# Optimization experiments

Hardware: AMD Instinct MI355X
Metric: run time of the kernel (lower is better)

## Reference

```python
import jax, jax.numpy as jnp
import numpy as np

IMG = 128; P = 16; ND = IMG // P; N = ND * ND  # 64 patches
INF = 3 * P * P      # 768 flattened patch features
ATT = 768; HID = 3072; OUT = 768; B = 64
EPS = 1e-5


def setup_inputs() -> dict:
    key = jax.random.key(0)
    ks = jax.random.split(key, 24)
    w = lambda k, shape: jax.random.normal(k, shape, jnp.float32) * 0.02
    return {
        "x": jax.random.normal(ks[0], (B, 3, IMG, IMG), jnp.float32),
        # per-patch q/k/v projections: [n, in, out] weights, [n, out] biases
        "Wq": w(ks[1], (N, INF, ATT)), "bq": w(ks[2], (N, ATT)),
        "Wk": w(ks[3], (N, INF, ATT)), "bk": w(ks[4], (N, ATT)),
        "Wv": w(ks[5], (N, INF, ATT)), "bv": w(ks[6], (N, ATT)),
        "ln_g": jnp.ones((ATT,), jnp.float32), "ln_b": jnp.zeros((ATT,), jnp.float32),
        "p1_w": w(ks[7], (INF, ATT)), "p1_b": w(ks[8], (ATT,)),
        "w0": w(ks[9], (ATT, HID)),  "b0": w(ks[10], (HID,)),
        "w1": w(ks[11], (HID, HID)), "b1": w(ks[12], (HID,)),
        "w2": w(ks[13], (HID, HID)), "b2": w(ks[14], (HID,)),
        "w3": w(ks[15], (HID, HID)), "b3": w(ks[16], (HID,)),
        "w4": w(ks[17], (HID, OUT)), "b4": w(ks[18], (OUT,)),
        "p2_w": w(ks[19], (ATT, OUT)), "p2_b": w(ks[20], (OUT,)),
    }


def _forward(x, Wq, bq, Wk, bk, Wv, bv, ln_g, ln_b, p1_w, p1_b,
             w0, b0, w1, b1, w2, b2, w3, b3, w4, b4, p2_w, p2_b):
    b_ = x.shape[0]
    # patch split (row-major over (i,j) blocks) then flatten channel*patch dims
    flat = x.reshape(b_, 3, ND, P, ND, P).transpose(0, 2, 4, 1, 3, 5).reshape(b_, N, INF)
    # per-patch projections, attention taken ACROSS the batch dim (as in source)
    q = jnp.einsum('bnf,nfd->bnd', flat, Wq) + bq
    k = jnp.einsum('bnf,nfd->bnd', flat, Wk) + bk
    v = jnp.einsum('bnf,nfd->bnd', flat, Wv) + bv
    scores = jnp.einsum('bnd,cnd->nbc', q, k) / jnp.sqrt(jnp.float32(ATT))  # [n,B,B]
    attn = jnp.einsum('nbc,cnd->bnd', jax.nn.softmax(scores, axis=-1), v)  # [B,n,ATT]
    # LayerNorm(att_features)
    mu = attn.mean(-1, keepdims=True)
    var = ((attn - mu) ** 2).mean(-1, keepdims=True)
    ln = (attn - mu) / jnp.sqrt(var + EPS) * ln_g + ln_b
    att = ln + flat @ p1_w + p1_b
    # linear stack (no nonlinearity in the source)
    h = att @ w0 + b0
    h = h @ w1 + b1
    h = h @ w2 + b2
    h = h @ w3 + b3
    h = h @ w4 + b4
    proj = h + att @ p2_w + p2_b
    return jax.nn.softmax(proj, axis=2)


def reference(x, Wq, bq, Wk, bk, Wv, bv, ln_g, ln_b, p1_w, p1_b,
              w0, b0, w1, b1, w2, b2, w3, b3, w4, b4, p2_w, p2_b):
    return _forward(x, Wq, bq, Wk, bk, Wv, bv, ln_g, ln_b, p1_w, p1_b,
                    w0, b0, w1, b1, w2, b2, w3, b3, w4, b4, p2_w, p2_b)
```

## Files before the change

kernel.cpp:

```cpp
#include <hip/hip_runtime.h>
#include <hip/hip_bf16.h>

using bf16 = __bf16;
using bf16x4 = __bf16 __attribute__((ext_vector_type(4)));
using bf16x8 = __bf16 __attribute__((ext_vector_type(8)));
using f32x4 = float __attribute__((ext_vector_type(4)));

static constexpr long ROWEL = 64L * 768;

__global__ __launch_bounds__(256) void k_patchify(const float* __restrict__ x, bf16* __restrict__ flat)
{
    const int n = blockIdx.x;
    const int b = blockIdx.y;
    const int i_ = n >> 3, j_ = n & 7;
    for (int it = 0; it < 3; ++it) {
        int f = threadIdx.x + it * 256;
        int c = f >> 8, rem = f & 255, pi = rem >> 4, pj = rem & 15;
        float v = x[(((long)(b * 3 + c)) << 14) + ((i_ * 16 + pi) << 7) + (j_ * 16 + pj)];
        flat[(long)b * ROWEL + n * 768 + f] = (bf16)v;
    }
}

__global__ __launch_bounds__(256) void k_cvt_t2(
    const float* __restrict__ W0, bf16* __restrict__ T0,
    const float* __restrict__ W1, bf16* __restrict__ T1)
{
    const int z = blockIdx.z;
    const float* W = z ? W1 : W0;
    bf16* Wt = z ? T1 : T0;
    const int Kd = z ? 768 : 3072, Nd = 768;
    if (z && blockIdx.x >= 12) return;
    __shared__ bf16 T[64 * 66];
    const int k0 = blockIdx.x * 64, n0 = blockIdx.y * 64;
    const int tid = threadIdx.x;
    const int kr = tid >> 4, nc = (tid & 15) * 4;
#pragma unroll
    for (int i = 0; i < 4; ++i) {
        f32x4 v = *(const f32x4*)(W + (long)(k0 + kr + i * 16) * Nd + n0 + nc);
#pragma unroll
        for (int e = 0; e < 4; ++e)
            T[(kr + i * 16) * 66 + nc + e] = (bf16)v[e];
    }
    __syncthreads();
    const int nr = tid >> 3, ks = (tid & 7) * 8;
#pragma unroll
    for (int it = 0; it < 2; ++it) {
        int n = nr + it * 32;
        bf16x8 o;
#pragma unroll
        for (int j = 0; j < 8; ++j) o[j] = T[(ks + j) * 66 + n];
        *(bf16x8*)(Wt + (long)(n0 + n) * Kd + k0 + ks) = o;
    }
}

__global__ __launch_bounds__(256) void k_cast4(
    const float* __restrict__ s0, bf16* __restrict__ d0,
    const float* __restrict__ s1, bf16* __restrict__ d1,
    const float* __restrict__ s2, bf16* __restrict__ d2,
    const float* __restrict__ s3, bf16* __restrict__ d3)
{
    const int z = blockIdx.y;
    const float* W = z == 0 ? s0 : z == 1 ? s1 : z == 2 ? s2 : s3;
    bf16* o = z == 0 ? d0 : z == 1 ? d1 : z == 2 ? d2 : d3;
    const long nelem = z == 0 ? 768L * 3072 : 3072L * 3072;
    long i = ((long)blockIdx.x * 256 + threadIdx.x) * 8;
    if (i >= nelem) return;
    f32x4 a = *(const f32x4*)(W + i);
    f32x4 b = *(const f32x4*)(W + i + 4);
    bf16x8 v;
#pragma unroll
    for (int e = 0; e < 4; ++e) { v[e] = (bf16)a[e]; v[4 + e] = (bf16)b[e]; }
    *(bf16x8*)(o + i) = v;
}

__device__ __forceinline__ void barrier_lgkm()
{
    asm volatile("s_waitcnt lgkmcnt(0)" ::: "memory");
    __builtin_amdgcn_s_barrier();
    __builtin_amdgcn_sched_barrier(0);
}

template<int BM, int BN>
__global__ __launch_bounds__(256) void k_gemm_rs(
    const bf16* __restrict__ A, long lda,
    const bf16* __restrict__ Bt, long ldb,
    int Ks,
    const float* __restrict__ bias,
    const float* __restrict__ addm,
    bf16* __restrict__ Cb, float* __restrict__ Cf, long ldc,
    float* __restrict__ Cp, long zstride)
{
    constexpr int WM = BM / 2, WN = BN / 2, FM = WM / 16, FN = WN / 16;
    constexpr int NA = BM / 64, NB = BN / 64;
    __shared__ bf16 As[2][BM * 32];
    __shared__ bf16 Bs[2][BN * 32];
    const int tid = threadIdx.x, lane = tid & 63, wave = tid >> 6;
    const int wm = wave >> 1, wn = wave & 1;
    const long m0 = (long)blockIdx.x * BM, n0 = (long)blockIdx.y * BN;
    const long kofs = (long)blockIdx.z * Ks;

    f32x4 acc[FM][FN];
#pragma unroll
    for (int i = 0; i < FM; ++i)
#pragma unroll
        for (int j = 0; j < FN; ++j) acc[i][j] = (f32x4){0.f, 0.f, 0.f, 0.f};

    const int nk = Ks >> 5;
    bf16x8 Xa[NA], Xb[NB], Ya[NA], Yb[NB];

    auto LOAD = [&](bf16x8 (&ra)[NA], bf16x8 (&rb)[NB], int kt) {
        const long kb = kofs + (long)kt * 32;
#pragma unroll
        for (int i = 0; i < NA; ++i) {
            const int c = i * 256 + tid, r = c >> 2, sg = c & 3;
            ra[i] = *(const bf16x8*)(A + (m0 + r) * lda + kb + sg * 8);
        }
#pragma unroll
        for (int i = 0; i < NB; ++i) {
            const int c = i * 256 + tid, r = c >> 2, sg = c & 3;
            rb[i] = *(const bf16x8*)(Bt + (n0 + r) * ldb + kb + sg * 8);
        }
    };
    auto WRITE = [&](bf16x8 (&ra)[NA], bf16x8 (&rb)[NB], int buf) {
#pragma unroll
        for (int i = 0; i < NA; ++i)
            *(bf16x8*)&As[buf][(i * 256 + tid) * 8] = ra[i];
#pragma unroll
        for (int i = 0; i < NB; ++i)
            *(bf16x8*)&Bs[buf][(i * 256 + tid) * 8] = rb[i];
    };
    auto COMPUTE = [&](int buf) {
        bf16x8 af[FM], bfr[FN];
#pragma unroll
        for (int i = 0; i < FM; ++i)
            af[i] = *(const bf16x8*)&As[buf][(wm * WM + i * 16 + (lane & 15)) * 32 + (lane >> 4) * 8];
#pragma unroll
        for (int j = 0; j < FN; ++j)
            bfr[j] = *(const bf16x8*)&Bs[buf][(wn * WN + j * 16 + (lane & 15)) * 32 + (lane >> 4) * 8];
#pragma unroll
        for (int i = 0; i < FM; ++i)
#pragma unroll
            for (int j = 0; j < FN; ++j)
                acc[i][j] = __builtin_amdgcn_mfma_f32_16x16x32_bf16(af[i], bfr[j], acc[i][j], 0, 0, 0);
    };

    LOAD(Xa, Xb, 0);
    LOAD(Ya, Yb, 1);
    WRITE(Xa, Xb, 0);
    barrier_lgkm();
    for (int t = 0; t < nk; t += 2) {
        if (t + 2 < nk) LOAD(Xa, Xb, t + 2);
        COMPUTE(0);
        if (t + 1 < nk) WRITE(Ya, Yb, 1);
        barrier_lgkm();
        if (t + 1 < nk) {
            if (t + 3 < nk) LOAD(Ya, Yb, t + 3);
            COMPUTE(1);
            if (t + 2 < nk) WRITE(Xa, Xb, 0);
            barrier_lgkm();
        }
    }

    if (Cp) {
        float* Cz = Cp + (long)blockIdx.z * zstride;
#pragma unroll
        for (int j = 0; j < FN; ++j) {
            const long col = n0 + wn * WN + j * 16 + (lane & 15);
#pragma unroll
            for (int i = 0; i < FM; ++i)
#pragma unroll
                for (int r = 0; r < 4; ++r) {
                    const long row = m0 + wm * WM + i * 16 + (lane >> 4) * 4 + r;
                    Cz[row * ldc + col] = acc[i][j][r];
                }
        }
        return;
    }
#pragma unroll
    for (int j = 0; j < FN; ++j) {
        const long col = n0 + wn * WN + j * 16 + (lane & 15);
        const float bb = bias ? bias[col] : 0.f;
#pragma unroll
        for (int i = 0; i < FM; ++i) {
#pragma unroll
            for (int r = 0; r < 4; ++r) {
                const long row = m0 + wm * WM + i * 16 + (lane >> 4) * 4 + r;
                const long idx = row * ldc + col;
                float v = acc[i][j][r] + bb;
                if (addm) v += addm[idx];
                if (Cb) Cb[idx] = (bf16)v;
                if (Cf) Cf[idx] = v;
            }
        }
    }
}

__global__ __launch_bounds__(256) void k_qkv(
    const bf16* __restrict__ flat,
    const float* __restrict__ Wq, const float* __restrict__ Wk, const float* __restrict__ Wv,
    const float* __restrict__ bq, const float* __restrict__ bk, const float* __restrict__ bv,
    bf16* __restrict__ qo, bf16* __restrict__ ko, bf16* __restrict__ vo)
{
    const int zz = blockIdx.z;
    const float* W = zz == 0 ? Wq : zz == 1 ? Wk : Wv;
    const float* bias = zz == 0 ? bq : zz == 1 ? bk : bv;
    bf16* out = zz == 0 ? qo : zz == 1 ? ko : vo;

    __shared__ bf16 As[2][64 * 32];
    __shared__ bf16 Bs[2][64 * 32];
    const int tid = threadIdx.x, lane = tid & 63, wave = tid >> 6;
    const int wm = wave >> 1, wn = wave & 1;
    const int n0 = blockIdx.x * 64;
    const int z = blockIdx.y;
    const float* Wz = W + (long)z * 589824;

    f32x4 acc[2][2];
#pragma unroll
    for (int i = 0; i < 2; ++i)
#pragma unroll
        for (int j = 0; j < 2; ++j) acc[i][j] = (f32x4){0.f, 0.f, 0.f, 0.f};

    const int bcol = tid & 63;
    const int bkg = (tid >> 6) * 8;
    bf16x8 Xa, Ya;
    float Xb[8], Yb[8];

    auto LOAD = [&](bf16x8& ra, float (&rb)[8], int kt) {
        const int kb = kt * 32;
        const int r = tid >> 2, sg = tid & 3;
        ra = *(const bf16x8*)(flat + (long)r * ROWEL + z * 768 + kb + sg * 8);
#pragma unroll
        for (int e = 0; e < 8; ++e)
            rb[e] = Wz[(long)(kb + bkg + e) * 768 + n0 + bcol];
    };
    auto WRITE = [&](bf16x8& ra, float (&rb)[8], int buf) {
        *(bf16x8*)&As[buf][tid * 8] = ra;
        bf16x8 bb;
#pragma unroll
        for (int e = 0; e < 8; ++e) bb[e] = (bf16)rb[e];
        *(bf16x8*)&Bs[buf][bcol * 32 + bkg] = bb;
    };
    auto COMPUTE = [&](int buf) {
        bf16x8 af[2], bfr[2];
#pragma unroll
        for (int i = 0; i < 2; ++i)
            af[i] = *(const bf16x8*)&As[buf][(wm * 32 + i * 16 + (lane & 15)) * 32 + (lane >> 4) * 8];
#pragma unroll
        for (int j = 0; j < 2; ++j)
            bfr[j] = *(const bf16x8*)&Bs[buf][(wn * 32 + j * 16 + (lane & 15)) * 32 + (lane >> 4) * 8];
#pragma unroll
        for (int i = 0; i < 2; ++i)
#pragma unroll
            for (int j = 0; j < 2; ++j)
                acc[i][j] = __builtin_amdgcn_mfma_f32_16x16x32_bf16(af[i], bfr[j], acc[i][j], 0, 0, 0);
    };

    const int nk = 24;
    LOAD(Xa, Xb, 0);
    LOAD(Ya, Yb, 1);
    WRITE(Xa, Xb, 0);
    barrier_lgkm();
    for (int t = 0; t < nk; t += 2) {
        if (t + 2 < nk) LOAD(Xa, Xb, t + 2);
        COMPUTE(0);
        if (t + 1 < nk) WRITE(Ya, Yb, 1);
        barrier_lgkm();
        if (t + 1 < nk) {
            if (t + 3 < nk) LOAD(Ya, Yb, t + 3);
            COMPUTE(1);
            if (t + 2 < nk) WRITE(Xa, Xb, 0);
            barrier_lgkm();
        }
    }

#pragma unroll
    for (int j = 0; j < 2; ++j) {
        const int col = n0 + wn * 32 + j * 16 + (lane & 15);
        const float bb = bias[z * 768 + col];
#pragma unroll
        for (int i = 0; i < 2; ++i) {
#pragma unroll
            for (int r = 0; r < 4; ++r) {
                const int row = wm * 32 + i * 16 + (lane >> 4) * 4 + r;
                out[(long)row * ROWEL + z * 768 + col] = (bf16)(acc[i][j][r] + bb);
            }
        }
    }
}

__global__ __launch_bounds__(256) void k_skadd(
    const float* __restrict__ P, long zstride, int S, long nelem, bf16* __restrict__ out)
{
    long i = ((long)blockIdx.x * 256 + threadIdx.x) * 4;
    if (i >= nelem) return;
    f32x4 s = *(const f32x4*)(P + i);
    for (int z = 1; z < S; ++z) {
        f32x4 p = *(const f32x4*)(P + (long)z * zstride + i);
        s += p;
    }
    bf16x4 o;
#pragma unroll
    for (int e = 0; e < 4; ++e) o[e] = (bf16)s[e];
    *(bf16x4*)(out + i) = o;
}

__global__ __launch_bounds__(256) void k_skaddT(
    const float* __restrict__ P, long zstride, int S,
    const float* __restrict__ p2w, bf16* __restrict__ Mt)
{
    const int n = blockIdx.x;
    for (int k = threadIdx.x; k < 768; k += 256) {
        float s = p2w[(long)k * 768 + n];
        for (int z = 0; z < S; ++z) s += P[(long)z * zstride + n * 768 + k];
        Mt[n * 768 + k] = (bf16)s;
    }
}

template<typename TW>
__global__ __launch_bounds__(256) void k_vm2(
    const float* __restrict__ Pin, const float* __restrict__ bin, const TW* __restrict__ W,
    int K, int N, float* __restrict__ Pout)
{
    __shared__ float red[4][64];
    const int tid = threadIdx.x;
    const int nl = tid & 63, kq = tid >> 6;
    const int n = blockIdx.x * 64 + nl;
    const int kc = blockIdx.y;
    const int kchunk = K / 8, kslice = kchunk / 4;
    const int k0 = kc * kchunk + kq * kslice;
    float acc = 0.f;
#pragma unroll 4
    for (int k = k0; k < k0 + kslice; ++k) {
        float vk = bin[k];
        if (Pin) {
#pragma unroll
            for (int j = 0; j < 8; ++j) vk += Pin[(long)j * K + k];
        }
        acc += vk * (float)W[(long)k * N + n];
    }
    red[kq][nl] = acc;
    __syncthreads();
    if (kq == 0)
        Pout[(long)kc * N + n] = red[0][nl] + red[1][nl] + red[2][nl] + red[3][nl];
}

__global__ __launch_bounds__(256) void k_vred(
    const float* __restrict__ P, const float* __restrict__ b1, const float* __restrict__ b2,
    int N, float* __restrict__ out)
{
    const int n = blockIdx.x * 256 + threadIdx.x;
    if (n >= N) return;
    float s = b1[n] + (b2 ? b2[n] : 0.f);
#pragma unroll
    for (int j = 0; j < 8; ++j) s += P[(long)j * N + n];
    out[n] = s;
}

__global__ __launch_bounds__(256) void k_attn(
    const bf16* __restrict__ q, const bf16* __restrict__ k, const bf16* __restrict__ v,
    float* __restrict__ attn)
{
    const int dc = blockIdx.x;
    const int n = blockIdx.y;
    __shared__ bf16 QT[64 * 72];
    __shared__ bf16 KT[64 * 72];
    __shared__ float S[64 * 66];
    __shared__ bf16 P[64 * 72];
    __shared__ bf16 VT[128 * 72];

    const int tid = threadIdx.x, lane = tid & 63, wave = tid >> 6;
    const int wm = wave >> 1, wn = wave & 1;

    f32x4 accs[2][2];
#pragma unroll
    for (int i = 0; i < 2; ++i)
#pragma unroll
        for (int j = 0; j < 2; ++j) accs[i][j] = (f32x4){0.f, 0.f, 0.f, 0.f};

    for (int kt = 0; kt < 12; ++kt) {
#pragma unroll
        for (int i = 0; i < 2; ++i) {
            int cid = tid + i * 256;
            int r = cid >> 3, seg = cid & 7;
            *(bf16x8*)&QT[r * 72 + seg * 8] = *(const bf16x8*)(q + (long)r * ROWEL + n * 768 + kt * 64 + seg * 8);
            *(bf16x8*)&KT[r * 72 + seg * 8] = *(const bf16x8*)(k + (long)r * ROWEL + n * 768 + kt * 64 + seg * 8);
        }
        __syncthreads();
#pragma unroll
        for (int ks = 0; ks < 2; ++ks) {
            bf16x8 qa[2], kb2[2];
#pragma unroll
            for (int i = 0; i < 2; ++i)
                qa[i] = *(const bf16x8*)&QT[(wm * 32 + i * 16 + (lane & 15)) * 72 + ks * 32 + (lane >> 4) * 8];
#pragma unroll
            for (int j = 0; j < 2; ++j)
                kb2[j] = *(const bf16x8*)&KT[(wn * 32 + j * 16 + (lane & 15)) * 72 + ks * 32 + (lane >> 4) * 8];
#pragma unroll
            for (int i = 0; i < 2; ++i)
#pragma unroll
                for (int j = 0; j < 2; ++j)
                    accs[i][j] = __builtin_amdgcn_mfma_f32_16x16x32_bf16(qa[i], kb2[j], accs[i][j], 0, 0, 0);
        }
        __syncthreads();
    }
    const float sc = 0.03608439182435161f;
#pragma unroll
    for (int i = 0; i < 2; ++i)
#pragma unroll
        for (int j = 0; j < 2; ++j)
#pragma unroll
            for (int r = 0; r < 4; ++r)
                S[(wm * 32 + i * 16 + (lane >> 4) * 4 + r) * 66 + wn * 32 + j * 16 + (lane & 15)] = accs[i][j][r] * sc;
    __syncthreads();

    {
        int r = tid >> 2, l4 = tid & 3;
        float m = -1e30f;
        for (int c = l4; c < 64; c += 4) m = fmaxf(m, S[r * 66 + c]);
        m = fmaxf(m, __shfl_xor(m, 1));
        m = fmaxf(m, __shfl_xor(m, 2));
        float s = 0.f;
// ... 61 lines not shown
    for (int c = 0; c < 3; ++c) {
        xv[c] = *(const f32x4*)(p + c * 256 + lane * 4);
        s += xv[c][0] + xv[c][1] + xv[c][2] + xv[c][3];
    }
#pragma unroll
    for (int o = 1; o < 64; o <<= 1) s += __shfl_xor(s, o);
    const float mu = s * (1.f / 768.f);
    float vs = 0.f;
#pragma unroll
    for (int c = 0; c < 3; ++c)
#pragma unroll
        for (int e = 0; e < 4; ++e) { float d = xv[c][e] - mu; vs += d * d; }
#pragma unroll
    for (int o = 1; o < 64; o <<= 1) vs += __shfl_xor(vs, o);
    const float rstd = rsqrtf(vs * (1.f / 768.f) + 1e-5f);
#pragma unroll
    for (int c = 0; c < 3; ++c)
#pragma unroll
        for (int e = 0; e < 4; ++e) {
            int col = c * 256 + lane * 4 + e;
            p[col] = (xv[c][e] - mu) * rstd * g[col] + bb[col];
        }
}

__global__ __launch_bounds__(256) void k_softmax(float* __restrict__ o)
{
    const long row = blockIdx.x * 4 + (threadIdx.x >> 6);
    const int lane = threadIdx.x & 63;
    float* p = o + row * 768;
    f32x4 xv[3];
    float m = -1e30f;
#pragma unroll
    for (int c = 0; c < 3; ++c) {
        xv[c] = *(const f32x4*)(p + c * 256 + lane * 4);
        m = fmaxf(m, fmaxf(fmaxf(xv[c][0], xv[c][1]), fmaxf(xv[c][2], xv[c][3])));
    }
#pragma unroll
    for (int o2 = 1; o2 < 64; o2 <<= 1) m = fmaxf(m, __shfl_xor(m, o2));
    float s = 0.f;
#pragma unroll
    for (int c = 0; c < 3; ++c)
#pragma unroll
        for (int e = 0; e < 4; ++e) { float ev = __expf(xv[c][e] - m); xv[c][e] = ev; s += ev; }
#pragma unroll
    for (int o2 = 1; o2 < 64; o2 <<= 1) s += __shfl_xor(s, o2);
    const float inv = 1.f / s;
#pragma unroll
    for (int c = 0; c < 3; ++c)
        *(f32x4*)(p + c * 256 + lane * 4) = xv[c] * inv;
}

extern "C" void kernel_launch(void* const* d_in, const int* in_sizes, int n_in,
                              void* d_out, int out_size, void* d_ws, size_t ws_size,
                              hipStream_t stream)
{
    const float* x   = (const float*)d_in[0];
    const float* Wq  = (const float*)d_in[1];
    const float* bq  = (const float*)d_in[2];
    const float* Wk  = (const float*)d_in[3];
    const float* bk  = (const float*)d_in[4];
    const float* Wv  = (const float*)d_in[5];
    const float* bv  = (const float*)d_in[6];
    const float* lng = (const float*)d_in[7];
    const float* lnb = (const float*)d_in[8];
    const float* p1w = (const float*)d_in[9];
    const float* p1b = (const float*)d_in[10];
    const float* w0  = (const float*)d_in[11];
    const float* b0  = (const float*)d_in[12];
    const float* w1  = (const float*)d_in[13];
    const float* b1  = (const float*)d_in[14];
    const float* w2  = (const float*)d_in[15];
    const float* b2  = (const float*)d_in[16];
    const float* w3  = (const float*)d_in[17];
    const float* b3  = (const float*)d_in[18];
    const float* w4  = (const float*)d_in[19];
    const float* b4  = (const float*)d_in[20];
    const float* p2w = (const float*)d_in[21];
    const float* p2b = (const float*)d_in[22];
    float* out = (float*)d_out;

    char* wsbase = (char*)d_ws;
    size_t off = 0;
    auto alloc = [&](size_t bytes) { char* p = wsbase + off; off += (bytes + 255) & ~(size_t)255; return p; };
    bf16*  flat = (bf16*)alloc(4096L * 768 * 2);
    bf16*  qb   = (bf16*)alloc(4096L * 768 * 2);
    bf16*  kb   = (bf16*)alloc(4096L * 768 * 2);
    bf16*  vb2  = (bf16*)alloc(4096L * 768 * 2);
    float* attn = (float*)alloc(4096L * 768 * 4);
    bf16*  att  = (bf16*)alloc(4096L * 768 * 2);
    bf16*  p1t  = (bf16*)alloc(768L * 768 * 2);
    bf16*  w4t  = (bf16*)alloc(768L * 3072 * 2);
    bf16*  w0c  = (bf16*)alloc(768L * 3072 * 2);
    bf16*  w1c  = (bf16*)alloc(3072L * 3072 * 2);
    bf16*  w2c  = (bf16*)alloc(3072L * 3072 * 2);
    bf16*  w3c  = (bf16*)alloc(3072L * 3072 * 2);
    bf16*  M1   = (bf16*)alloc(768L * 3072 * 2);
    bf16*  M2   = (bf16*)alloc(768L * 3072 * 2);
    bf16*  M3   = (bf16*)alloc(768L * 3072 * 2);
    bf16*  Mt   = (bf16*)alloc(768L * 768 * 2);
    float* Cp   = (float*)alloc(6L * 768 * 3072 * 4);
    float* vPa  = (float*)alloc(8L * 3072 * 4);
    float* vPb  = (float*)alloc(8L * 3072 * 4);
    float* c4   = (float*)alloc(768 * 4);
    if (off > ws_size) return;

    const long ZS = 768L * 3072;
    const long ZS4 = 768L * 768;

    k_patchify<<<dim3(64, 64), 256, 0, stream>>>(x, flat);
    k_cast4<<<dim3(4608, 4), 256, 0, stream>>>(w0, w0c, w1, w1c, w2, w2c, w3, w3c);
    k_cvt_t2<<<dim3(48, 12, 2), 256, 0, stream>>>(w4, w4t, p1w, p1t);

    k_qkv<<<dim3(12, 64, 3), 256, 0, stream>>>(flat, Wq, Wk, Wv, bq, bk, bv, qb, kb, vb2);

    k_attn<<<dim3(6, 64), 256, 0, stream>>>(qb, kb, vb2, attn);
    k_ln<<<1024, 256, 0, stream>>>(attn, lng, lnb);
    k_gemm_rs<64, 64><<<dim3(64, 12), 256, 0, stream>>>(flat, 768, p1t, 768, 768, p1b, attn, att, nullptr, 768, nullptr, 0);

    k_gemm_rs<64, 64><<<dim3(12, 48, 3), 256, 0, stream>>>(w4t, 3072, w3c, 3072, 1024, nullptr, nullptr, nullptr, nullptr, 3072, Cp, ZS);
    k_skadd<<<2304, 256, 0, stream>>>(Cp, ZS, 3, ZS, M1);
    k_gemm_rs<64, 64><<<dim3(12, 48, 3), 256, 0, stream>>>(M1, 3072, w2c, 3072, 1024, nullptr, nullptr, nullptr, nullptr, 3072, Cp, ZS);
    k_skadd<<<2304, 256, 0, stream>>>(Cp, ZS, 3, ZS, M2);
    k_gemm_rs<64, 64><<<dim3(12, 48, 3), 256, 0, stream>>>(M2, 3072, w1c, 3072, 1024, nullptr, nullptr, nullptr, nullptr, 3072, Cp, ZS);
    k_skadd<<<2304, 256, 0, stream>>>(Cp, ZS, 3, ZS, M3);
    k_gemm_rs<64, 64><<<dim3(12, 12, 6), 256, 0, stream>>>(M3, 3072, w0c, 3072, 512, nullptr, nullptr, nullptr, nullptr, 768, Cp, ZS4);
    k_skaddT<<<768, 256, 0, stream>>>(Cp, ZS4, 6, p2w, Mt);

    k_vm2<bf16><<<dim3(48, 8), 256, 0, stream>>>(nullptr, b0, w1c, 3072, 3072, vPa);
    k_vm2<bf16><<<dim3(48, 8), 256, 0, stream>>>(vPa, b1, w2c, 3072, 3072, vPb);
    k_vm2<bf16><<<dim3(48, 8), 256, 0, stream>>>(vPb, b2, w3c, 3072, 3072, vPa);
    k_vm2<float><<<dim3(12, 8), 256, 0, stream>>>(vPa, b3, w4, 3072, 768, vPb);
    k_vred<<<3, 256, 0, stream>>>(vPb, b4, p2b, 768, c4);

    k_gemm_rs<64, 64><<<dim3(64, 12), 256, 0, stream>>>(att, 768, Mt, 768, 768, c4, nullptr, nullptr, out, 768, nullptr, 0);
    k_softmax<<<1024, 256, 0, stream>>>(out);
}
```

Before: 577.5 us.

## Fuse weight casts and split-K reductions into chained GEMM loads with XCD-aware block mapping

Measured after the change: 684.7 us. +18.6%, slower.

```diff
diff --git a/kernel.cpp b/kernel.cpp
--- a/kernel.cpp
+++ b/kernel.cpp
@@ -53,26 +53,6 @@
     }
 }
 
-__global__ __launch_bounds__(256) void k_cast4(
-    const float* __restrict__ s0, bf16* __restrict__ d0,
-    const float* __restrict__ s1, bf16* __restrict__ d1,
-    const float* __restrict__ s2, bf16* __restrict__ d2,
-    const float* __restrict__ s3, bf16* __restrict__ d3)
-{
-    const int z = blockIdx.y;
-    const float* W = z == 0 ? s0 : z == 1 ? s1 : z == 2 ? s2 : s3;
-    bf16* o = z == 0 ? d0 : z == 1 ? d1 : z == 2 ? d2 : d3;
-    const long nelem = z == 0 ? 768L * 3072 : 3072L * 3072;
-    long i = ((long)blockIdx.x * 256 + threadIdx.x) * 8;
-    if (i >= nelem) return;
-    f32x4 a = *(const f32x4*)(W + i);
-    f32x4 b = *(const f32x4*)(W + i + 4);
-    bf16x8 v;
-#pragma unroll
-    for (int e = 0; e < 4; ++e) { v[e] = (bf16)a[e]; v[4 + e] = (bf16)b[e]; }
-    *(bf16x8*)(o + i) = v;
-}
-
 __device__ __forceinline__ void barrier_lgkm()
 {
     asm volatile("s_waitcnt lgkmcnt(0)" ::: "memory");
@@ -87,8 +67,7 @@
     int Ks,
     const float* __restrict__ bias,
     const float* __restrict__ addm,
-    bf16* __restrict__ Cb, float* __restrict__ Cf, long ldc,
-    float* __restrict__ Cp, long zstride)
+    bf16* __restrict__ Cb, float* __restrict__ Cf, long ldc)
 {
     constexpr int WM = BM / 2, WN = BN / 2, FM = WM / 16, FN = WN / 16;
     constexpr int NA = BM / 64, NB = BN / 64;
@@ -97,7 +76,6 @@
     const int tid = threadIdx.x, lane = tid & 63, wave = tid >> 6;
     const int wm = wave >> 1, wn = wave & 1;
     const long m0 = (long)blockIdx.x * BM, n0 = (long)blockIdx.y * BN;
-    const long kofs = (long)blockIdx.z * Ks;
 
     f32x4 acc[FM][FN];
 #pragma unroll
@@ -109,7 +87,7 @@
     bf16x8 Xa[NA], Xb[NB], Ya[NA], Yb[NB];
 
     auto LOAD = [&](bf16x8 (&ra)[NA], bf16x8 (&rb)[NB], int kt) {
-        const long kb = kofs + (long)kt * 32;
+        const long kb = (long)kt * 32;
 #pragma unroll
         for (int i = 0; i < NA; ++i) {
             const int c = i * 256 + tid, r = c >> 2, sg = c & 3;
@@ -161,21 +139,6 @@
         }
     }
 
-    if (Cp) {
-        float* Cz = Cp + (long)blockIdx.z * zstride;
-#pragma unroll
-        for (int j = 0; j < FN; ++j) {
-            const long col = n0 + wn * WN + j * 16 + (lane & 15);
-#pragma unroll
-            for (int i = 0; i < FM; ++i)
-#pragma unroll
-                for (int r = 0; r < 4; ++r) {
-                    const long row = m0 + wm * WM + i * 16 + (lane >> 4) * 4 + r;
-                    Cz[row * ldc + col] = acc[i][j][r];
-                }
-        }
-        return;
-    }
 #pragma unroll
     for (int j = 0; j < FN; ++j) {
         const long col = n0 + wn * WN + j * 16 + (lane & 15);
@@ -195,24 +158,151 @@
     }
 }
 
+template<bool ASUM>
+__global__ __launch_bounds__(256) void k_chain(
+    const bf16* __restrict__ Abf, const float* __restrict__ Ap, long apz, long lda,
+    const float* __restrict__ Bf, long ldb,
+    int Ks, int NX, int NY,
+    float* __restrict__ Cp, long zstride, long ldc)
+{
+    constexpr int BM = 64, BN = 64;
+    constexpr int WM = 32, WN = 32, FM = 2, FN = 2;
+    __shared__ bf16 As[2][BM * 32];
+    __shared__ bf16 Bs[2][BN * 32];
+    const int tid = threadIdx.x, lane = tid & 63, wave = tid >> 6;
+    const int wm = wave >> 1, wn = wave & 1;
+    const int gid = blockIdx.x;
+    const int xcd = gid & 7, mm = gid >> 3;
+    const int bx = mm % NX, u = mm / NX;
+    const int p = 8 * u + xcd;
+    const int by = p % NY, bz = p / NY;
+    const long m0 = (long)bx * BM, n0 = (long)by * BN;
+    const long kofs = (long)bz * Ks;
+
+    f32x4 acc[FM][FN];
+#pragma unroll
+    for (int i = 0; i < FM; ++i)
+#pragma unroll
+        for (int j = 0; j < FN; ++j) acc[i][j] = (f32x4){0.f, 0.f, 0.f, 0.f};
+
+    const int nk = Ks >> 5;
+
+    bf16x8 XaB, YaB;
+    f32x4 Xa[2][3], Ya[2][3];
+    f32x4 Xb[2], Yb[2];
+
+    auto LOAD = [&](bf16x8& raB, f32x4 (&ra)[2][3], f32x4 (&rb)[2], int kt) {
+        const long kb = kofs + (long)kt * 32;
+        if (ASUM) {
+#pragma unroll
+            for (int i = 0; i < 2; ++i) {
+                const int c = i * 256 + tid, r = c >> 3, k4 = (c & 7) * 4;
+#pragma unroll
+                for (int z = 0; z < 3; ++z)
+                    ra[i][z] = *(const f32x4*)(Ap + (long)z * apz + (m0 + r) * lda + kb + k4);
+            }
+        } else {
+            const int r = tid >> 2, sg = tid & 3;
+            raB = *(const bf16x8*)(Abf + (m0 + r) * lda + kb + sg * 8);
+        }
+#pragma unroll
+        for (int i = 0; i < 2; ++i) {
+            const int c = i * 256 + tid, n = c >> 3, k4 = (c & 7) * 4;
+            rb[i] = *(const f32x4*)(Bf + (n0 + n) * ldb + kb + k4);
+        }
+    };
+    auto WRITE = [&](bf16x8& raB, f32x4 (&ra)[2][3], f32x4 (&rb)[2], int buf) {
+        if (ASUM) {
+#pragma unroll
+            for (int i = 0; i < 2; ++i) {
+                const int c = i * 256 + tid, r = c >> 3, k4 = (c & 7) * 4;
+                f32x4 s = ra[i][0] + ra[i][1] + ra[i][2];
+                bf16x4 o;
+#pragma unroll
+                for (int e = 0; e < 4; ++e) o[e] = (bf16)s[e];
+                *(bf16x4*)&As[buf][r * 32 + k4] = o;
+            }
+        } else {
+            *(bf16x8*)&As[buf][tid * 8] = raB;
+        }
+#pragma unroll
+        for (int i = 0; i < 2; ++i) {
+            const int c = i * 256 + tid, n = c >> 3, k4 = (c & 7) * 4;
+            bf16x4 o;
+#pragma unroll
+            for (int e = 0; e < 4; ++e) o[e] = (bf16)rb[i][e];
+            *(bf16x4*)&Bs[buf][n * 32 + k4] = o;
+        }
+    };
+    auto COMPUTE = [&](int buf) {
+        bf16x8 af[FM], bfr[FN];
+#pragma unroll
+        for (int i = 0; i < FM; ++i)
+            af[i] = *(const bf16x8*)&As[buf][(wm * WM + i * 16 + (lane & 15)) * 32 + (lane >> 4) * 8];
+#pragma unroll
+        for (int j = 0; j < FN; ++j)
+            bfr[j] = *(const bf16x8*)&Bs[buf][(wn * WN + j * 16 + (lane & 15)) * 32 + (lane >> 4) * 8];
+#pragma unroll
+        for (int i = 0; i < FM; ++i)
+#pragma unroll
+            for (int j = 0; j < FN; ++j)
+                acc[i][j] = __builtin_amdgcn_mfma_f32_16x16x32_bf16(af[i], bfr[j], acc[i][j], 0, 0, 0);
+    };
+
+    LOAD(XaB, Xa, Xb, 0);
+    LOAD(YaB, Ya, Yb, 1);
+    WRITE(XaB, Xa, Xb, 0);
+    barrier_lgkm();
+    for (int t = 0; t < nk; t += 2) {
+        if (t + 2 < nk) LOAD(XaB, Xa, Xb, t + 2);
+        COMPUTE(0);
+        if (t + 1 < nk) WRITE(YaB, Ya, Yb, 1);
+        barrier_lgkm();
+        if (t + 1 < nk) {
+            if (t + 3 < nk) LOAD(YaB, Ya, Yb, t + 3);
+            COMPUTE(1);
+            if (t + 2 < nk) WRITE(XaB, Xa, Xb, 0);
+            barrier_lgkm();
+        }
+    }
+
+    float* Cz = Cp + (long)bz * zstride;
+#pragma unroll
+    for (int j = 0; j < FN; ++j) {
+        const long col = n0 + wn * WN + j * 16 + (lane & 15);
+#pragma unroll
+        for (int i = 0; i < FM; ++i)
+#pragma unroll
+            for (int r = 0; r < 4; ++r) {
+                const long row = m0 + wm * WM + i * 16 + (lane >> 4) * 4 + r;
+                Cz[row * ldc + col] = acc[i][j][r];
+            }
+    }
+}
+
 __global__ __launch_bounds__(256) void k_qkv(
     const bf16* __restrict__ flat,
     const float* __restrict__ Wq, const float* __restrict__ Wk, const float* __restrict__ Wv,
     const float* __restrict__ bq, const float* __restrict__ bk, const float* __restrict__ bv,
     bf16* __restrict__ qo, bf16* __restrict__ ko, bf16* __restrict__ vo)
 {
-    const int zz = blockIdx.z;
-    const float* W = zz == 0 ? Wq : zz == 1 ? Wk : Wv;
-    const float* bias = zz == 0 ? bq : zz == 1 ? bk : bv;
-    bf16* out = zz == 0 ? qo : zz == 1 ? ko : vo;
+    const int gid = blockIdx.x;
+    const int xcd = gid & 7, mm = gid >> 3;
+    const int nt = mm % 12, u = mm / 12;
+    const int p = 8 * u + xcd;
+    const int z = p >> 6;
+    const int zp = p & 63;
+
+    const float* W = z == 0 ? Wq : z == 1 ? Wk : Wv;
+    const float* bias = z == 0 ? bq : z == 1 ? bk : bv;
+    bf16* out = z == 0 ? qo : z == 1 ? ko : vo;
 
     __shared__ bf16 As[2][64 * 32];
     __shared__ bf16 Bs[2][64 * 32];
     const int tid = threadIdx.x, lane = tid & 63, wave = tid >> 6;
     const int wm = wave >> 1, wn = wave & 1;
-    const int n0 = blockIdx.x * 64;
-    const int z = blockIdx.y;
-    const float* Wz = W + (long)z * 589824;
+    const int n0 = nt * 64;
+    const float* Wz = W + (long)zp * 589824;
 
     f32x4 acc[2][2];
 #pragma unroll
@@ -222,25 +312,25 @@
 
     const int bcol = tid & 63;
     const int bkg = (tid >> 6) * 8;
-    bf16x8 Xa, Ya;
-    float Xb[8], Yb[8];
-
-    auto LOAD = [&](bf16x8& ra, float (&rb)[8], int kt) {
+    bf16x8 A0, A1, A2, A3;
+    float B0[8], B1[8], B2[8], B3[8];
+
+    auto LOADQ = [&](bf16x8& ra, float (&rb)[8], int kt) {
         const int kb = kt * 32;
         const int r = tid >> 2, sg = tid & 3;
-        ra = *(const bf16x8*)(flat + (long)r * ROWEL + z * 768 + kb + sg * 8);
+        ra = *(const bf16x8*)(flat + (long)r * ROWEL + zp * 768 + kb + sg * 8);
 #pragma unroll
         for (int e = 0; e < 8; ++e)
             rb[e] = Wz[(long)(kb + bkg + e) * 768 + n0 + bcol];
     };
-    auto WRITE = [&](bf16x8& ra, float (&rb)[8], int buf) {
+    auto WRITEQ = [&](bf16x8& ra, float (&rb)[8], int buf) {
         *(bf16x8*)&As[buf][tid * 8] = ra;
         bf16x8 bb;
 #pragma unroll
         for (int e = 0; e < 8; ++e) bb[e] = (bf16)rb[e];
         *(bf16x8*)&Bs[buf][bcol * 32 + bkg] = bb;
     };
-    auto COMPUTE = [&](int buf) {
+    auto COMPUTEQ = [&](int buf) {
         bf16x8 af[2], bfr[2];
 #pragma unroll
         for (int i = 0; i < 2; ++i)
@@ -256,52 +346,43 @@
     };
 
     const int nk = 24;
-    LOAD(Xa, Xb, 0);
-    LOAD(Ya, Yb, 1);
-    WRITE(Xa, Xb, 0);
+    LOADQ(A0, B0, 0);
+    LOADQ(A1, B1, 1);
+    LOADQ(A2, B2, 2);
+    WRITEQ(A0, B0, 0);
     barrier_lgkm();
-    for (int t = 0; t < nk; t += 2) {
-        if (t + 2 < nk) LOAD(Xa, Xb, t + 2);
-        COMPUTE(0);
-        if (t + 1 < nk) WRITE(Ya, Yb, 1);
+    for (int t = 0; t < nk; t += 4) {
+        if (t + 3 < nk) LOADQ(A3, B3, t + 3);
+        COMPUTEQ(0);
+        WRITEQ(A1, B1, 1);
         barrier_lgkm();
-        if (t + 1 < nk) {
-            if (t + 3 < nk) LOAD(Ya, Yb, t + 3);
-            COMPUTE(1);
-            if (t + 2 < nk) WRITE(Xa, Xb, 0);
-            barrier_lgkm();
-        }
+        if (t + 4 < nk) LOADQ(A0, B0, t + 4);
+        COMPUTEQ(1);
+        WRITEQ(A2, B2, 0);
+        barrier_lgkm();
+        if (t + 5 < nk) LOADQ(A1, B1, t + 5);
+        COMPUTEQ(0);
+        WRITEQ(A3, B3, 1);
+        barrier_lgkm();
+        if (t + 6 < nk) LOADQ(A2, B2, t + 6);
+        COMPUTEQ(1);
+        if (t + 4 < nk) WRITEQ(A0, B0, 0);
+        barrier_lgkm();
     }
 
 #pragma unroll
     for (int j = 0; j < 2; ++j) {
         const int col = n0 + wn * 32 + j * 16 + (lane & 15);
-        const float bb = bias[z * 768 + col];
+        const float bb = bias[zp * 768 + col];
 #pragma unroll
         for (int i = 0; i < 2; ++i) {
 #pragma unroll
             for (int r = 0; r < 4; ++r) {
                 const int row = wm * 32 + i * 16 + (lane >> 4) * 4 + r;
-                out[(long)row * ROWEL + z * 768 + col] = (bf16)(acc[i][j][r] + bb);
+                out[(long)row * ROWEL + zp * 768 + col] = (bf16)(acc[i][j][r] + bb);
             }
         }
     }
-}
-
-__global__ __launch_bounds__(256) void k_skadd(
-    const float* __restrict__ P, long zstride, int S, long nelem, bf16* __restrict__ out)
-{
-    long i = ((long)blockIdx.x * 256 + threadIdx.x) * 4;
-    if (i >= nelem) return;
-    f32x4 s = *(const f32x4*)(P + i);
-    for (int z = 1; z < S; ++z) {
-        f32x4 p = *(const f32x4*)(P + (long)z * zstride + i);
-        s += p;
-    }
-    bf16x4 o;
-#pragma unroll
-    for (int e = 0; e < 4; ++e) o[e] = (bf16)s[e];
-    *(bf16x4*)(out + i) = o;
 }
 
 __global__ __launch_bounds__(256) void k_skaddT(
@@ -316,9 +397,8 @@
     }
 }
 
-template<typename TW>
 __global__ __launch_bounds__(256) void k_vm2(
-    const float* __restrict__ Pin, const float* __restrict__ bin, const TW* __restrict__ W,
+    const float* __restrict__ Pin, const float* __restrict__ bin, const float* __restrict__ W,
     int K, int N, float* __restrict__ Pout)
 {
     __shared__ float red[4][64];
@@ -336,7 +416,7 @@
 #pragma unroll
             for (int j = 0; j < 8; ++j) vk += Pin[(long)j * K + k];
         }
-        acc += vk * (float)W[(long)k * N + n];
+        acc += vk * W[(long)k * N + n];
     }
     red[kq][nl] = acc;
     __syncthreads();
@@ -572,48 +652,38 @@
     bf16*  att  = (bf16*)alloc(4096L * 768 * 2);
     bf16*  p1t  = (bf16*)alloc(768L * 768 * 2);
     bf16*  w4t  = (bf16*)alloc(768L * 3072 * 2);
-    bf16*  w0c  = (bf16*)alloc(768L * 3072 * 2);
-    bf16*  w1c  = (bf16*)alloc(3072L * 3072 * 2);
-    bf16*  w2c  = (bf16*)alloc(3072L * 3072 * 2);
-    bf16*  w3c  = (bf16*)alloc(3072L * 3072 * 2);
-    bf16*  M1   = (bf16*)alloc(768L * 3072 * 2);
-    bf16*  M2   = (bf16*)alloc(768L * 3072 * 2);
-    bf16*  M3   = (bf16*)alloc(768L * 3072 * 2);
     bf16*  Mt   = (bf16*)alloc(768L * 768 * 2);
-    float* Cp   = (float*)alloc(6L * 768 * 3072 * 4);
+    float* Cpa  = (float*)alloc(3L * 768 * 3072 * 4);
+    float* Cpb  = (float*)alloc(6L * 768 * 768 * 4 > 3L * 768 * 3072 * 4 ? 6L * 768 * 768 * 4 : 3L * 768 * 3072 * 4);
     float* vPa  = (float*)alloc(8L * 3072 * 4);
     float* vPb  = (float*)alloc(8L * 3072 * 4);
     float* c4   = (float*)alloc(768 * 4);
     if (off > ws_size) return;
 
-    const long ZS = 768L * 3072;
+    const long ZS  = 768L * 3072;
     const long ZS4 = 768L * 768;
 
     k_patchify<<<dim3(64, 64), 256, 0, stream>>>(x, flat);
-    k_cast4<<<dim3(4608, 4), 256, 0, stream>>>(w0, w0c, w1, w1c, w2, w2c, w3, w3c);
     k_cvt_t2<<<dim3(48, 12, 2), 256, 0, stream>>>(w4, w4t, p1w, p1t);
 
-    k_qkv<<<dim3(12, 64, 3), 256, 0, stream>>>(flat, Wq, Wk, Wv, bq, bk, bv, qb, kb, vb2);
+    k_qkv<<<2304, 256, 0, stream>>>(flat, Wq, Wk, Wv, bq, bk, bv, qb, kb, vb2);
 
     k_attn<<<dim3(6, 64), 256, 0, stream>>>(qb, kb, vb2, attn);
     k_ln<<<1024, 256, 0, stream>>>(attn, lng, lnb);
-    k_gemm_rs<64, 64><<<dim3(64, 12), 256, 0, stream>>>(flat, 768, p1t, 768, 768, p1b, attn, att, nullptr, 768, nullptr, 0);
-
-    k_gemm_rs<64, 64><<<dim3(12, 48, 3), 256, 0, stream>>>(w4t, 3072, w3c, 3072, 1024, nullptr, nullptr, nullptr, nullptr, 3072, Cp, ZS);
-    k_skadd<<<2304, 256, 0, stream>>>(Cp, ZS, 3, ZS, M1);
-    k_gemm_rs<64, 64><<<dim3(12, 48, 3), 256, 0, stream>>>(M1, 3072, w2c, 3072, 1024, nullptr, nullptr, nullptr, nullptr, 3072, Cp, ZS);
-    k_skadd<<<2304, 256, 0, stream>>>(Cp, ZS, 3, ZS, M2);
-    k_gemm_rs<64, 64><<<dim3(12, 48, 3), 256, 0, stream>>>(M2, 3072, w1c, 3072, 1024, nullptr, nullptr, nullptr, nullptr, 3072, Cp, ZS);
-    k_skadd<<<2304, 256, 0, stream>>>(Cp, ZS, 3, ZS, M3);
-    k_gemm_rs<64, 64><<<dim3(12, 12, 6), 256, 0, stream>>>(M3, 3072, w0c, 3072, 512, nullptr, nullptr, nullptr, nullptr, 768, Cp, ZS4);
-    k_skaddT<<<768, 256, 0, stream>>>(Cp, ZS4, 6, p2w, Mt);
-
-    k_vm2<bf16><<<dim3(48, 8), 256, 0, stream>>>(nullptr, b0, w1c, 3072, 3072, vPa);
-    k_vm2<bf16><<<dim3(48, 8), 256, 0, stream>>>(vPa, b1, w2c, 3072, 3072, vPb);
-    k_vm2<bf16><<<dim3(48, 8), 256, 0, stream>>>(vPb, b2, w3c, 3072, 3072, vPa);
-    k_vm2<float><<<dim3(12, 8), 256, 0, stream>>>(vPa, b3, w4, 3072, 768, vPb);
+    k_gemm_rs<64, 64><<<dim3(64, 12), 256, 0, stream>>>(flat, 768, p1t, 768, 768, p1b, attn, att, nullptr, 768);
+
+    k_chain<false><<<1728, 256, 0, stream>>>(w4t, nullptr, 0, 3072, w3, 3072, 1024, 12, 48, Cpa, ZS, 3072);
+    k_chain<true><<<1728, 256, 0, stream>>>(nullptr, Cpa, ZS, 3072, w2, 3072, 1024, 12, 48, Cpb, ZS, 3072);
+    k_chain<true><<<1728, 256, 0, stream>>>(nullptr, Cpb, ZS, 3072, w1, 3072, 1024, 12, 48, Cpa, ZS, 3072);
+    k_chain<true><<<864, 256, 0, stream>>>(nullptr, Cpa, ZS, 3072, w0, 3072, 512, 12, 12, Cpb, ZS4, 768);
+    k_skaddT<<<768, 256, 0, stream>>>(Cpb, ZS4, 6, p2w, Mt);
+
+    k_vm2<<<dim3(48, 8), 256, 0, stream>>>(nullptr, b0, w1, 3072, 3072, vPa);
+    k_vm2<<<dim3(48, 8), 256, 0, stream>>>(vPa, b1, w2, 3072, 3072, vPb);
+    k_vm2<<<dim3(48, 8), 256, 0, stream>>>(vPb, b2, w3, 3072, 3072, vPa);
+    k_vm2<<<dim3(12, 8), 256, 0, stream>>>(vPa, b3, w4, 3072, 768, vPb);
     k_vred<<<3, 256, 0, stream>>>(vPb, b4, p2b, 768, c4);
 
-    k_gemm_rs<64, 64><<<dim3(64, 12), 256, 0, stream>>>(att, 768, Mt, 768, 768, c4, nullptr, nullptr, out, 768, nullptr, 0);
+    k_gemm_rs<64, 64><<<dim3(64, 12), 256, 0, stream>>>(att, 768, Mt, 768, 768, c4, nullptr, nullptr, out, 768);
     k_softmax<<<1024, 256, 0, stream>>>(out);
 }
```

## Add patch-major flat copy, XCD-aware QKV scheduling, and fewer split-K slices

Applied to the files above, without the earlier changes.

Measured after the change: 556.7 us. -3.6%, faster.

```diff
diff --git a/kernel.cpp b/kernel.cpp
--- a/kernel.cpp
+++ b/kernel.cpp
@@ -8,7 +8,8 @@
 
 static constexpr long ROWEL = 64L * 768;
 
-__global__ __launch_bounds__(256) void k_patchify(const float* __restrict__ x, bf16* __restrict__ flat)
+__global__ __launch_bounds__(256) void k_patchify(const float* __restrict__ x,
+                                                  bf16* __restrict__ flat, bf16* __restrict__ flat_nb)
 {
     const int n = blockIdx.x;
     const int b = blockIdx.y;
@@ -17,7 +18,9 @@
         int f = threadIdx.x + it * 256;
         int c = f >> 8, rem = f & 255, pi = rem >> 4, pj = rem & 15;
         float v = x[(((long)(b * 3 + c)) << 14) + ((i_ * 16 + pi) << 7) + (j_ * 16 + pj)];
-        flat[(long)b * ROWEL + n * 768 + f] = (bf16)v;
+        bf16 o = (bf16)v;
+        flat[(long)b * ROWEL + n * 768 + f] = o;
+        flat_nb[(long)n * ROWEL + b * 768 + f] = o;
     }
 }
 
@@ -87,8 +90,7 @@
     int Ks,
     const float* __restrict__ bias,
     const float* __restrict__ addm,
-    bf16* __restrict__ Cb, float* __restrict__ Cf, long ldc,
-    float* __restrict__ Cp, long zstride)
+    bf16* __restrict__ Cb, float* __restrict__ Cf, long ldc)
 {
     constexpr int WM = BM / 2, WN = BN / 2, FM = WM / 16, FN = WN / 16;
     constexpr int NA = BM / 64, NB = BN / 64;
@@ -97,7 +99,6 @@
     const int tid = threadIdx.x, lane = tid & 63, wave = tid >> 6;
     const int wm = wave >> 1, wn = wave & 1;
     const long m0 = (long)blockIdx.x * BM, n0 = (long)blockIdx.y * BN;
-    const long kofs = (long)blockIdx.z * Ks;
 
     f32x4 acc[FM][FN];
 #pragma unroll
@@ -109,7 +110,7 @@
     bf16x8 Xa[NA], Xb[NB], Ya[NA], Yb[NB];
 
     auto LOAD = [&](bf16x8 (&ra)[NA], bf16x8 (&rb)[NB], int kt) {
-        const long kb = kofs + (long)kt * 32;
+        const long kb = (long)kt * 32;
 #pragma unroll
         for (int i = 0; i < NA; ++i) {
             const int c = i * 256 + tid, r = c >> 2, sg = c & 3;
@@ -161,21 +162,6 @@
         }
     }
 
-    if (Cp) {
-        float* Cz = Cp + (long)blockIdx.z * zstride;
-#pragma unroll
-        for (int j = 0; j < FN; ++j) {
-            const long col = n0 + wn * WN + j * 16 + (lane & 15);
-#pragma unroll
-            for (int i = 0; i < FM; ++i)
-#pragma unroll
-                for (int r = 0; r < 4; ++r) {
-                    const long row = m0 + wm * WM + i * 16 + (lane >> 4) * 4 + r;
-                    Cz[row * ldc + col] = acc[i][j][r];
-                }
-        }
-        return;
-    }
 #pragma unroll
     for (int j = 0; j < FN; ++j) {
         const long col = n0 + wn * WN + j * 16 + (lane & 15);
@@ -195,24 +181,18 @@
     }
 }
 
-__global__ __launch_bounds__(256) void k_qkv(
-    const bf16* __restrict__ flat,
-    const float* __restrict__ Wq, const float* __restrict__ Wk, const float* __restrict__ Wv,
-    const float* __restrict__ bq, const float* __restrict__ bk, const float* __restrict__ bv,
-    bf16* __restrict__ qo, bf16* __restrict__ ko, bf16* __restrict__ vo)
-{
-    const int zz = blockIdx.z;
-    const float* W = zz == 0 ? Wq : zz == 1 ? Wk : Wv;
-    const float* bias = zz == 0 ? bq : zz == 1 ? bk : bv;
-    bf16* out = zz == 0 ? qo : zz == 1 ? ko : vo;
-
+__global__ __launch_bounds__(256) void k_chainrs(
+    const bf16* __restrict__ A, long lda,
+    const bf16* __restrict__ Bt, long ldb,
+    int Ks,
+    float* __restrict__ Cp, long zstride, long ldc)
+{
     __shared__ bf16 As[2][64 * 32];
     __shared__ bf16 Bs[2][64 * 32];
     const int tid = threadIdx.x, lane = tid & 63, wave = tid >> 6;
     const int wm = wave >> 1, wn = wave & 1;
-    const int n0 = blockIdx.x * 64;
-    const int z = blockIdx.y;
-    const float* Wz = W + (long)z * 589824;
+    const long m0 = (long)blockIdx.x * 64, n0 = (long)blockIdx.y * 64;
+    const long kofs = (long)blockIdx.z * Ks;
 
     f32x4 acc[2][2];
 #pragma unroll
@@ -220,25 +200,18 @@
 #pragma unroll
         for (int j = 0; j < 2; ++j) acc[i][j] = (f32x4){0.f, 0.f, 0.f, 0.f};
 
-    const int bcol = tid & 63;
-    const int bkg = (tid >> 6) * 8;
-    bf16x8 Xa, Ya;
-    float Xb[8], Yb[8];
-
-    auto LOAD = [&](bf16x8& ra, float (&rb)[8], int kt) {
-        const int kb = kt * 32;
+    const int nk = Ks >> 5;
+    bf16x8 Xa, Xb, Ya, Yb;
+
+    auto LOAD = [&](bf16x8& ra, bf16x8& rb, int kt) {
+        const long kb = kofs + (long)kt * 32;
         const int r = tid >> 2, sg = tid & 3;
-        ra = *(const bf16x8*)(flat + (long)r * ROWEL + z * 768 + kb + sg * 8);
-#pragma unroll
-        for (int e = 0; e < 8; ++e)
-            rb[e] = Wz[(long)(kb + bkg + e) * 768 + n0 + bcol];
-    };
-    auto WRITE = [&](bf16x8& ra, float (&rb)[8], int buf) {
+        ra = *(const bf16x8*)(A + (m0 + r) * lda + kb + sg * 8);
+        rb = *(const bf16x8*)(Bt + (n0 + r) * ldb + kb + sg * 8);
+    };
+    auto WRITE = [&](bf16x8& ra, bf16x8& rb, int buf) {
         *(bf16x8*)&As[buf][tid * 8] = ra;
-        bf16x8 bb;
-#pragma unroll
-        for (int e = 0; e < 8; ++e) bb[e] = (bf16)rb[e];
-        *(bf16x8*)&Bs[buf][bcol * 32 + bkg] = bb;
+        *(bf16x8*)&Bs[buf][tid * 8] = rb;
     };
     auto COMPUTE = [&](int buf) {
         bf16x8 af[2], bfr[2];
@@ -255,7 +228,6 @@
                 acc[i][j] = __builtin_amdgcn_mfma_f32_16x16x32_bf16(af[i], bfr[j], acc[i][j], 0, 0, 0);
     };
 
-    const int nk = 24;
     LOAD(Xa, Xb, 0);
     LOAD(Ya, Yb, 1);
     WRITE(Xa, Xb, 0);
@@ -273,16 +245,114 @@
         }
     }
 
+    float* Cz = Cp + (long)blockIdx.z * zstride;
+#pragma unroll
+    for (int j = 0; j < 2; ++j) {
+        const long col = n0 + wn * 32 + j * 16 + (lane & 15);
+#pragma unroll
+        for (int i = 0; i < 2; ++i)
+#pragma unroll
+            for (int r = 0; r < 4; ++r) {
+                const long row = m0 + wm * 32 + i * 16 + (lane >> 4) * 4 + r;
+                Cz[row * ldc + col] = acc[i][j][r];
+            }
+    }
+}
+
+__global__ __launch_bounds__(256) void k_qkv(
+    const bf16* __restrict__ flat_nb,
+    const float* __restrict__ Wq, const float* __restrict__ Wk, const float* __restrict__ Wv,
+    const float* __restrict__ bq, const float* __restrict__ bk, const float* __restrict__ bv,
+    bf16* __restrict__ qo, bf16* __restrict__ ko, bf16* __restrict__ vo)
+{
+    const int gid = blockIdx.x;
+    const int xcd = gid & 7, mm = gid >> 3;
+    const int nt = mm % 12, u = mm / 12;
+    const int p = 8 * u + xcd;
+    const int z = p >> 6;
+    const int zp = p & 63;
+
+    const float* W = z == 0 ? Wq : z == 1 ? Wk : Wv;
+    const float* bias = z == 0 ? bq : z == 1 ? bk : bv;
+    bf16* out = z == 0 ? qo : z == 1 ? ko : vo;
+
+    __shared__ bf16 As[2][64 * 32];
+    __shared__ bf16 Bs[2][64 * 32];
+    const int tid = threadIdx.x, lane = tid & 63, wave = tid >> 6;
+    const int wm = wave >> 1, wn = wave & 1;
+    const int n0 = nt * 64;
+    const float* Wz = W + (long)zp * 589824;
+    const bf16* Az = flat_nb + (long)zp * ROWEL;
+
+    f32x4 acc[2][2];
+#pragma unroll
+    for (int i = 0; i < 2; ++i)
+#pragma unroll
+        for (int j = 0; j < 2; ++j) acc[i][j] = (f32x4){0.f, 0.f, 0.f, 0.f};
+
+    const int bcol = tid & 63;
+    const int bkg = (tid >> 6) * 8;
+    bf16x8 Xa, Ya;
+    float Xb[8], Yb[8];
+
+    auto LOADQ = [&](bf16x8& ra, float (&rb)[8], int kt) {
+        const int kb = kt * 32;
+        const int r = tid >> 2, sg = tid & 3;
+        ra = *(const bf16x8*)(Az + (long)r * 768 + kb + sg * 8);
+#pragma unroll
+        for (int e = 0; e < 8; ++e)
+            rb[e] = Wz[(long)(kb + bkg + e) * 768 + n0 + bcol];
+    };
+    auto WRITEQ = [&](bf16x8& ra, float (&rb)[8], int buf) {
+        *(bf16x8*)&As[buf][tid * 8] = ra;
+        bf16x8 bb;
+#pragma unroll
+        for (int e = 0; e < 8; ++e) bb[e] = (bf16)rb[e];
+        *(bf16x8*)&Bs[buf][bcol * 32 + bkg] = bb;
+    };
+    auto COMPUTEQ = [&](int buf) {
+        bf16x8 af[2], bfr[2];
+#pragma unroll
+        for (int i = 0; i < 2; ++i)
+            af[i] = *(const bf16x8*)&As[buf][(wm * 32 + i * 16 + (lane & 15)) * 32 + (lane >> 4) * 8];
+#pragma unroll
+        for (int j = 0; j < 2; ++j)
+            bfr[j] = *(const bf16x8*)&Bs[buf][(wn * 32 + j * 16 + (lane & 15)) * 32 + (lane >> 4) * 8];
+#pragma unroll
+        for (int i = 0; i < 2; ++i)
+#pragma unroll
+            for (int j = 0; j < 2; ++j)
+                acc[i][j] = __builtin_amdgcn_mfma_f32_16x16x32_bf16(af[i], bfr[j], acc[i][j], 0, 0, 0);
+    };
+
+    const int nk = 24;
+    LOADQ(Xa, Xb, 0);
+    LOADQ(Ya, Yb, 1);
+    WRITEQ(Xa, Xb, 0);
+    barrier_lgkm();
+    for (int t = 0; t < nk; t += 2) {
+        if (t + 2 < nk) LOADQ(Xa, Xb, t + 2);
+        COMPUTEQ(0);
+        if (t + 1 < nk) WRITEQ(Ya, Yb, 1);
+        barrier_lgkm();
+        if (t + 1 < nk) {
+            if (t + 3 < nk) LOADQ(Ya, Yb, t + 3);
+            COMPUTEQ(1);
+            if (t + 2 < nk) WRITEQ(Xa, Xb, 0);
+            barrier_lgkm();
+        }
+    }
+
 #pragma unroll
     for (int j = 0; j < 2; ++j) {
         const int col = n0 + wn * 32 + j * 16 + (lane & 15);
-        const float bb = bias[z * 768 + col];
+        const float bb = bias[zp * 768 + col];
 #pragma unroll
         for (int i = 0; i < 2; ++i) {
 #pragma unroll
             for (int r = 0; r < 4; ++r) {
                 const int row = wm * 32 + i * 16 + (lane >> 4) * 4 + r;
-                out[(long)row * ROWEL + z * 768 + col] = (bf16)(acc[i][j][r] + bb);
+                out[(long)row * ROWEL + zp * 768 + col] = (bf16)(acc[i][j][r] + bb);
             }
         }
     }
@@ -564,7 +634,8 @@
     char* wsbase = (char*)d_ws;
     size_t off = 0;
     auto alloc = [&](size_t bytes) { char* p = wsbase + off; off += (bytes + 255) & ~(size_t)255; return p; };
-    bf16*  flat = (bf16*)alloc(4096L * 768 * 2);
+    bf16*  flat    = (bf16*)alloc(4096L * 768 * 2);
+    bf16*  flat_nb = (bf16*)alloc(4096L * 768 * 2);
     bf16*  qb   = (bf16*)alloc(4096L * 768 * 2);
     bf16*  kb   = (bf16*)alloc(4096L * 768 * 2);
     bf16*  vb2  = (bf16*)alloc(4096L * 768 * 2);
@@ -580,33 +651,33 @@
     bf16*  M2   = (bf16*)alloc(768L * 3072 * 2);
     bf16*  M3   = (bf16*)alloc(768L * 3072 * 2);
     bf16*  Mt   = (bf16*)alloc(768L * 768 * 2);
-    float* Cp   = (float*)alloc(6L * 768 * 3072 * 4);
+    float* Cp   = (float*)alloc(4L * 768 * 3072 * 4);
     float* vPa  = (float*)alloc(8L * 3072 * 4);
     float* vPb  = (float*)alloc(8L * 3072 * 4);
     float* c4   = (float*)alloc(768 * 4);
     if (off > ws_size) return;
 
-    const long ZS = 768L * 3072;
+    const long ZS  = 768L * 3072;
     const long ZS4 = 768L * 768;
 
-    k_patchify<<<dim3(64, 64), 256, 0, stream>>>(x, flat);
+    k_patchify<<<dim3(64, 64), 256, 0, stream>>>(x, flat, flat_nb);
     k_cast4<<<dim3(4608, 4), 256, 0, stream>>>(w0, w0c, w1, w1c, w2, w2c, w3, w3c);
     k_cvt_t2<<<dim3(48, 12, 2), 256, 0, stream>>>(w4, w4t, p1w, p1t);
 
-    k_qkv<<<dim3(12, 64, 3), 256, 0, stream>>>(flat, Wq, Wk, Wv, bq, bk, bv, qb, kb, vb2);
+    k_qkv<<<2304, 256, 0, stream>>>(flat_nb, Wq, Wk, Wv, bq, bk, bv, qb, kb, vb2);
 
     k_attn<<<dim3(6, 64), 256, 0, stream>>>(qb, kb, vb2, attn);
     k_ln<<<1024, 256, 0, stream>>>(attn, lng, lnb);
-    k_gemm_rs<64, 64><<<dim3(64, 12), 256, 0, stream>>>(flat, 768, p1t, 768, 768, p1b, attn, att, nullptr, 768, nullptr, 0);
-
-    k_gemm_rs<64, 64><<<dim3(12, 48, 3), 256, 0, stream>>>(w4t, 3072, w3c, 3072, 1024, nullptr, nullptr, nullptr, nullptr, 3072, Cp, ZS);
-    k_skadd<<<2304, 256, 0, stream>>>(Cp, ZS, 3, ZS, M1);
-    k_gemm_rs<64, 64><<<dim3(12, 48, 3), 256, 0, stream>>>(M1, 3072, w2c, 3072, 1024, nullptr, nullptr, nullptr, nullptr, 3072, Cp, ZS);
-    k_skadd<<<2304, 256, 0, stream>>>(Cp, ZS, 3, ZS, M2);
-    k_gemm_rs<64, 64><<<dim3(12, 48, 3), 256, 0, stream>>>(M2, 3072, w1c, 3072, 1024, nullptr, nullptr, nullptr, nullptr, 3072, Cp, ZS);
-    k_skadd<<<2304, 256, 0, stream>>>(Cp, ZS, 3, ZS, M3);
-    k_gemm_rs<64, 64><<<dim3(12, 12, 6), 256, 0, stream>>>(M3, 3072, w0c, 3072, 512, nullptr, nullptr, nullptr, nullptr, 768, Cp, ZS4);
-    k_skaddT<<<768, 256, 0, stream>>>(Cp, ZS4, 6, p2w, Mt);
+    k_gemm_rs<64, 64><<<dim3(64, 12), 256, 0, stream>>>(flat, 768, p1t, 768, 768, p1b, attn, att, nullptr, 768);
+
+    k_chainrs<<<dim3(12, 48, 2), 256, 0, stream>>>(w4t, 3072, w3c, 3072, 1536, Cp, ZS, 3072);
+    k_skadd<<<2304, 256, 0, stream>>>(Cp, ZS, 2, ZS, M1);
+    k_chainrs<<<dim3(12, 48, 2), 256, 0, stream>>>(M1, 3072, w2c, 3072, 1536, Cp, ZS, 3072);
+    k_skadd<<<2304, 256, 0, stream>>>(Cp, ZS, 2, ZS, M2);
+    k_chainrs<<<dim3(12, 48, 2), 256, 0, stream>>>(M2, 3072, w1c, 3072, 1536, Cp, ZS, 3072);
+    k_skadd<<<2304, 256, 0, stream>>>(Cp, ZS, 2, ZS, M3);
+    k_chainrs<<<dim3(12, 12, 4), 256, 0, stream>>>(M3, 3072, w0c, 3072, 768, Cp, ZS4, 768);
+    k_skaddT<<<768, 256, 0, stream>>>(Cp, ZS4, 4, p2w, Mt);
 
     k_vm2<bf16><<<dim3(48, 8), 256, 0, stream>>>(nullptr, b0, w1c, 3072, 3072, vPa);
     k_vm2<bf16><<<dim3(48, 8), 256, 0, stream>>>(vPa, b1, w2c, 3072, 3072, vPb);
@@ -614,6 +685,6 @@
     k_vm2<float><<<dim3(12, 8), 256, 0, stream>>>(vPa, b3, w4, 3072, 768, vPb);
     k_vred<<<3, 256, 0, stream>>>(vPb, b4, p2b, 768, c4);
 
-    k_gemm_rs<64, 64><<<dim3(64, 12), 256, 0, stream>>>(att, 768, Mt, 768, 768, c4, nullptr, nullptr, out, 768, nullptr, 0);
+    k_gemm_rs<64, 64><<<dim3(64, 12), 256, 0, stream>>>(att, 768, Mt, 768, 768, c4, nullptr, nullptr, out, 768);
     k_softmax<<<1024, 256, 0, stream>>>(out);
 }
```
